# Performance work log

Hardware: AMD Instinct MI355X
Metric: run time of the kernel (lower is better)

## Reference

```python
import jax, jax.numpy as jnp
import numpy as np

# ---- module config (matches init_kwargs) ----
OGFH, OGFW = 256, 704
DOWNSAMPLE = 8
FH, FW = OGFH // DOWNSAMPLE, OGFW // DOWNSAMPLE   # 32, 88
DBOUND = (4.0, 45.0, 1.0)
D = int((DBOUND[1] - DBOUND[0]) / DBOUND[2])      # 41 depth bins
CAMC = 64
XB = (-50.0, 50.0, 0.5)    # lateral  -> nx = 200
YB = (-10.0, 10.0, 20.0)   # vertical -> ny = 1
ZB = (0.0, 50.0, 0.25)     # depth    -> nz = 200
NX = np.array([int((b[1] - b[0]) / b[2]) for b in (XB, YB, ZB)])  # [200, 1, 200]
DX = np.array([b[2] for b in (XB, YB, ZB)], dtype=np.float32)
BX = np.array([b[0] + b[2] / 2.0 for b in (XB, YB, ZB)], dtype=np.float32)


def make_frustum():
    # matches create_frustum_1camera: [D, fH, fW, 3] of (u, v, depth)
    ds = jnp.broadcast_to(
        jnp.arange(DBOUND[0], DBOUND[1], DBOUND[2], dtype=jnp.float32)[:, None, None],
        (D, FH, FW))
    xs = jnp.broadcast_to(
        jnp.linspace(0.0, OGFW - 1, FW, dtype=jnp.float32)[None, None, :], (D, FH, FW))
    ys = jnp.broadcast_to(
        jnp.linspace(0.0, OGFH - 1, FH, dtype=jnp.float32)[None, :, None], (D, FH, FW))
    return jnp.stack((xs, ys, ds), -1)


def setup_inputs() -> dict:
    key = jax.random.key(0)
    B = 4
    # depthnet output: first D channels = depth logits, next CAMC = context feats
    x = jax.random.normal(key, (B, D + CAMC, FH, FW), dtype=jnp.float32)
    fx = fy = 520.0
    K = jnp.array([[fx, 0.0, OGFW / 2.0],
                   [0.0, fy, OGFH / 2.0],
                   [0.0, 0.0, 1.0]], dtype=jnp.float32)
    intrins = jnp.broadcast_to(K, (B, 3, 3))
    post_rots = jnp.broadcast_to(jnp.eye(3, dtype=jnp.float32), (B, 3, 3))
    post_trans = jnp.zeros((B, 3), dtype=jnp.float32)
    return {"x": x, "intrins": intrins, "post_rots": post_rots, "post_trans": post_trans}


def _forward(x, intrins, post_rots, post_trans):
    B = x.shape[0]
    frustum = make_frustum()                                                     # [D,H,W,3]
    # ---- get_geometry ----
    pts = frustum[None] - post_trans[:, None, None, None, :]                     # [B,D,H,W,3]
    pts = jnp.einsum('bij,bdhwj->bdhwi', jnp.linalg.inv(post_rots), pts)
    pts = jnp.concatenate([pts[..., :2] * pts[..., 2:3], pts[..., 2:3]], -1)     # un-normalize
    geom = jnp.einsum('bij,bdhwj->bdhwi', jnp.linalg.inv(intrins), pts)          # [B,D,H,W,3]
    # ---- lift: depth softmax (x) context features ----
    depth = jax.nn.softmax(x[:, :D], axis=1)                                     # [B,D,H,W]
    feat = x[:, D:D + CAMC]                                                      # [B,C,H,W]
    vol = depth[:, None] * feat[:, :, None]                                      # [B,C,D,H,W]
    vol = jnp.transpose(vol, (0, 2, 3, 4, 1))                                    # [B,D,H,W,C]
    # ---- voxel_splat (sort+cumsum trick == segmented sum) ----
    Nprime = B * D * FH * FW
    feats = vol.reshape(Nprime, CAMC)
    # torch .long() truncates toward zero -> astype(int32)
    coords = ((geom - (BX - DX / 2.0)) / DX).astype(jnp.int32).reshape(Nprime, 3)
    bix = jnp.repeat(jnp.arange(B, dtype=jnp.int32), Nprime // B)
    kept = ((coords[:, 0] >= 0) & (coords[:, 0] < int(NX[0])) &
            (coords[:, 1] >= 0) & (coords[:, 1] < int(NX[1])) &
            (coords[:, 2] >= 0) & (coords[:, 2] < int(NX[2])))
    nseg = int(NX[0] * NX[1] * NX[2]) * B
    ranks = (coords[:, 0] * (int(NX[1]) * int(NX[2]) * B)
             + coords[:, 1] * (int(NX[2]) * B)
             + coords[:, 2] * B + bix)
    ranks = jnp.where(kept, ranks, nseg)  # dump bucket for dropped points
    pooled = jax.ops.segment_sum(jnp.where(kept[:, None], feats, 0.0), ranks,
                                 num_segments=nseg + 1)[:nseg]
    final = pooled.reshape(int(NX[0]), int(NX[1]), int(NX[2]), B, CAMC)          # [x,y,z,B,C]
    final = jnp.transpose(final, (3, 4, 1, 2, 0))                                # [B,C,ny,nz,nx]
    # torch.cat(final.unbind(dim=2), 1): collapse ny into channels (y-major)
    final = jnp.transpose(final, (0, 2, 1, 3, 4)).reshape(
        B, CAMC * int(NX[1]), int(NX[2]), int(NX[0]))                            # [B,C,200,200]
    return final


def reference(x, intrins, post_rots, post_trans):
    return _forward(x, intrins, post_rots, post_trans)
```

## Files before the change

kernel.cpp:

```cpp
#include <hip/hip_runtime.h>
#include <math.h>

#define DD   41
#define FHh  32
#define FWw  88
#define CC   64
#define CH   32
#define CG8  8
#define NXx  200
#define NZz  200
#define NCH  (DD + CC)
#define PLANE ((size_t)FHh * FWw)
#define NE   (DD * FWw)
#define DCAP 4
#define OVCAP 4096

__global__ __launch_bounds__(256) void lss_colpool(
    const float* __restrict__ x,
    const float* __restrict__ intrins,
    const float* __restrict__ post_rots,
    const float* __restrict__ post_trans,
    float* __restrict__ P, int* __restrict__ V,
    int* __restrict__ rowcnt8, int* __restrict__ ovcnt,
    float* __restrict__ out, int out_quads)
{
    __shared__ float Wt[DD][FHh + 1];
    __shared__ float F4s[FHh][36];
    __shared__ float Mi[18];
    __shared__ float pm[8][FHh + 1];
    __shared__ int   Vtmp[DD];

    int blk   = blockIdx.x;
    int chalf = blk & 1;
    int w     = (blk >> 1) % FWw;
    int b     = blk / (2 * FWw);
    int t     = threadIdx.x;
    const float* xb = x + (size_t)b * NCH * PLANE + w;

    for (int idx = t; idx < DD * FHh; idx += 256) {
        int d = idx >> 5, h = idx & 31;
        Wt[d][h] = xb[((size_t)d * FHh + h) * FWw];
    }
    for (int idx = t; idx < FHh * CH; idx += 256) {
        int c = idx & 31, h = idx >> 5;
        F4s[h][c] = xb[((size_t)(DD + chalf * CH + c) * FHh + h) * FWw];
    }
    if (t >= 64 && t < 64 + DD) Vtmp[t - 64] = -1;
    if (t == 0) {
        #pragma clang fp contract(off)
        for (int m = 0; m < 2; ++m) {
            const float* A = (m == 0 ? post_rots : intrins) + b * 9;
            float* O = Mi + m * 9;
            float a = A[0], bb = A[1], c = A[2];
            float d = A[3], e  = A[4], f = A[5];
            float g = A[6], h  = A[7], i = A[8];
            float det = a * (e * i - f * h) - bb * (d * i - f * g) + c * (d * h - e * g);
            O[0] = (e * i - f * h) / det;
            O[1] = (c * h - bb * i) / det;
            O[2] = (bb * f - c * e) / det;
            O[3] = (f * g - d * i) / det;
            O[4] = (a * i - c * g) / det;
            O[5] = (c * d - a * f) / det;
            O[6] = (d * h - e * g) / det;
            O[7] = (bb * g - a * h) / det;
            O[8] = (a * e - bb * d) / det;
        }
    }
    __syncthreads();

    int h = t & 31, l = t >> 5;
    float e_[6];
    {
        float pmax = -INFINITY;
        for (int d = l; d < DD; d += 8) pmax = fmaxf(pmax, Wt[d][h]);
        pm[l][h] = pmax;
    }
    __syncthreads();
    float mx = -INFINITY;
    for (int j = 0; j < 8; ++j) mx = fmaxf(mx, pm[j][h]);
    __syncthreads();
    {
        #pragma clang fp contract(off)
        float psum = 0.0f;
        int k = 0;
        for (int d = l; d < DD; d += 8, ++k) {
            float e = expf(Wt[d][h] - mx);
            e_[k] = e; psum += e;
        }
        pm[l][h] = psum;
    }
    __syncthreads();
    float s = 0.0f;
    for (int j = 0; j < 8; ++j) s += pm[j][h];

    {
        #pragma clang fp contract(off)
        float xs = (float)((double)w * 703.0 / 87.0);
        float ys = (float)((double)h * 255.0 / 31.0);
        float tx = post_trans[b * 3 + 0];
        float ty = post_trans[b * 3 + 1];
        float tz = post_trans[b * 3 + 2];
        int k = 0;
        for (int d = l; d < DD; d += 8, ++k) {
            float z  = 4.0f + (float)d;
            float px = xs - tx, py = ys - ty, pz = z - tz;
            float rx = Mi[0] * px + Mi[1] * py + Mi[2] * pz;
            float ry = Mi[3] * px + Mi[4] * py + Mi[5] * pz;
            float rz = Mi[6] * px + Mi[7] * py + Mi[8] * pz;
            float qx = rx * rz, qy = ry * rz, qz = rz;
            float gx = Mi[ 9] * qx + Mi[10] * qy + Mi[11] * qz;
            float gy = Mi[12] * qx + Mi[13] * qy + Mi[14] * qz;
            float gz = Mi[15] * qx + Mi[16] * qy + Mi[17] * qz;
            float cx = (gx + 50.0f) / 0.5f;
            float cy = (gy + 10.0f) / 20.0f;
            float cz = gz / 0.25f;
            int ix = (int)cx;
            int iy = (int)cy;
            int iz = (int)cz;
            bool kept = (ix >= 0) & (ix < NXx) & (iy == 0) & (iz >= 0) & (iz < NZz);
            if (kept) {
                Wt[d][h] = e_[k] / s;
                Vtmp[d] = iz * NXx + ix;
            } else {
                Wt[d][h] = 0.0f;
            }
        }
    }
    __syncthreads();

    float* Pb = P + ((size_t)b * NE) * CC + chalf * CH;
    {
        int c4 = t & 7;
        for (int d = t >> 3; d < DD; d += 32) {
            float4 acc = make_float4(0.f, 0.f, 0.f, 0.f);
            for (int hh = 0; hh < FHh; ++hh) {
                float wtv = Wt[d][hh];
                float4 fv = *(const float4*)&F4s[hh][c4 * 4];
                acc.x += wtv * fv.x; acc.y += wtv * fv.y;
                acc.z += wtv * fv.z; acc.w += wtv * fv.w;
            }
            *(float4*)&Pb[((size_t)d * FWw + w) * CC + c4 * 4] = acc;
        }
    }
    if (chalf == 0) {
        if (t < DD) V[(size_t)b * NE + (size_t)t * FWw + w] = Vtmp[t];
        if (w == 0) for (int i = t; i < NZz * 8; i += 256) rowcnt8[b * NZz * 8 + i] = 0;
    }
    if (blk == 0 && t == 0) *ovcnt = 0;

    {
        float4 z = make_float4(0.f, 0.f, 0.f, 0.f);
        float4* o4 = (float4*)out;
        int stride = gridDim.x * 256;
        for (int i = blk * 256 + t; i < out_quads; i += stride) o4[i] = z;
    }
}

__global__ __launch_bounds__(256) void lss_rowbuild(
    const float* __restrict__ P, const int* __restrict__ V,
    float* __restrict__ S, int* __restrict__ izd,
    int* __restrict__ rowcnt8, int* __restrict__ dlist8,
    int* __restrict__ ovcnt, int* __restrict__ ovlist,
    float* __restrict__ out)
{
    __shared__ float acc[CG8 * (NXx + 1)];
    __shared__ int ixw[FWw];
    __shared__ int izw[FWw];
    __shared__ int key;
    __shared__ int s_k;

    int blk = blockIdx.x;
    int cg = blk & 7;
    int bd = blk >> 3;
    int d = bd % DD;
    int b = bd / DD;
    int t = threadIdx.x;

    if (t == 0) key = 0x7fffffff;
    for (int i = t; i < CG8 * (NXx + 1); i += 256) acc[i] = 0.0f;
    __syncthreads();
    if (t < FWw) {
        int v = V[(size_t)bd * FWw + t];
        if (v >= 0) {
            int iz = v / NXx;
            izw[t] = iz; ixw[t] = v - iz * NXx;
            atomicMin(&key, (t << 16) | iz);
        } else { izw[t] = -1; ixw[t] = -1; }
    }
    __syncthreads();
    int kk = key;
    int s_iz = (kk == 0x7fffffff) ? -1 : (kk & 0xffff);
    if (cg == 0 && t == 0) izd[bd] = s_iz;
    if (s_iz < 0) return;

    int r = b * NZz + s_iz;
    if (t == 0) {
        int k = atomicAdd(&rowcnt8[r * 8 + cg], 1);
        if (k < DCAP) dlist8[(r * 8 + cg) * DCAP + k] = d;
        s_k = k;
    }
    if (cg == 0 && t < FWw && izw[t] >= 0 && izw[t] != s_iz) {
        int k = atomicAdd(ovcnt, 1);
        if (k < OVCAP)
            ovlist[k] = (b << 29) | (d << 23) | (t << 16) | (ixw[t] << 8) | izw[t];
    }

    const float* Pb = P + (size_t)bd * FWw * CC + cg * CG8;
    for (int idx = t; idx < FWw * 2; idx += 256) {
        int w = idx >> 1, q = idx & 1;
        if (izw[w] == s_iz) {
            float4 v = *(const float4*)&Pb[(size_t)w * CC + q * 4];
            int ix = ixw[w];
            int cb = q * 4;
            atomicAdd(&acc[(cb + 0) * (NXx + 1) + ix], v.x);
            atomicAdd(&acc[(cb + 1) * (NXx + 1) + ix], v.y);
            atomicAdd(&acc[(cb + 2) * (NXx + 1) + ix], v.z);
            atomicAdd(&acc[(cb + 3) * (NXx + 1) + ix], v.w);
        }
    }
    __syncthreads();

    bool owner0 = (s_k == 0);
    for (int i = t; i < CG8 * (NXx / 4); i += 256) {
        int c = i / (NXx / 4), q = i - c * (NXx / 4);
        int base = c * (NXx + 1) + q * 4;
        float4 vv;
        vv.x = acc[base + 0];
        vv.y = acc[base + 1];
        vv.z = acc[base + 2];
        vv.w = acc[base + 3];
        if (owner0) {
            float* orow = out + (((size_t)(b * CC + cg * CG8 + c)) * NZz + s_iz) * NXx;
            ((float4*)orow)[q] = vv;
        } else {
            float* Srow = S + ((size_t)bd * CC + cg * CG8 + c) * NXx;
            ((float4*)Srow)[q] = vv;
        }
    }
}

__global__ __launch_bounds__(256) void lss_fixup(
    const float* __restrict__ S, const int* __restrict__ izd,
    const int* __restrict__ rowcnt8, const int* __restrict__ dlist8,
    const float* __restrict__ P,
    const int* __restrict__ ovcnt, const int* __restrict__ ovlist,
    float* __restrict__ out)
{
    int b = blockIdx.x;
    int t = threadIdx.x;

    for (int pair = t; pair < NZz * 8; pair += 256) {
        int n = rowcnt8[b * NZz * 8 + pair];
        if (n <= 1) continue;
        int iz = pair >> 3, cg = pair & 7;
        const int* dl = dlist8 + (size_t)(b * NZz * 8 + pair) * DCAP;
        if (n <= DCAP) {
            for (int k = 1; k < n; ++k) {
                int d = dl[k];
                for (int c = 0; c < CG8; ++c) {
                    const float* Srow = S + ((size_t)(b * DD + d) * CC + cg * CG8 + c) * NXx;
                    float* orow = out + (((size_t)(b * CC + cg * CG8 + c)) * NZz + iz) * NXx;
                    for (int ix = 0; ix < NXx; ++ix) atomicAdd(&orow[ix], Srow[ix]);
                }
            }
        } else {
            int owner0 = dl[0];
            for (int d = 0; d < DD; ++d) {
                if (izd[b * DD + d] == iz && d != owner0) {
                    for (int c = 0; c < CG8; ++c) {
                        const float* Srow = S + ((size_t)(b * DD + d) * CC + cg * CG8 + c) * NXx;
                        float* orow = out + (((size_t)(b * CC + cg * CG8 + c)) * NZz + iz) * NXx;
                        for (int ix = 0; ix < NXx; ++ix) atomicAdd(&orow[ix], Srow[ix]);
                    }
                }
            }
        }
    }

    if (b == 0 && t == 0) {
        int nov = *ovcnt;
        if (nov > OVCAP) nov = OVCAP;
        for (int k = 0; k < nov; ++k) {
            int ent = ovlist[k];
            int eb  = (ent >> 29) & 7;
            int ed  = (ent >> 23) & 63;
            int ew  = (ent >> 16) & 127;
            int eix = (ent >> 8) & 255;
            int eiz = ent & 255;
            for (int c = 0; c < CC; ++c) {
                size_t o = (((size_t)(eb * CC + c)) * NZz + eiz) * NXx + eix;
                atomicAdd(&out[o], P[(((size_t)eb * DD + ed) * FWw + ew) * CC + c]);
            }
        }
    }
}

extern "C" void kernel_launch(void* const* d_in, const int* in_sizes, int n_in,
                              void* d_out, int out_size, void* d_ws, size_t ws_size,
                              hipStream_t stream)
{
    const float* x          = (const float*)d_in[0];
    const float* intrins    = (const float*)d_in[1];
    const float* post_rots  = (const float*)d_in[2];
    const float* post_trans = (const float*)d_in[3];
    float* out = (float*)d_out;

    int B = in_sizes[0] / (NCH * (int)PLANE);

    size_t off = 0;
    auto alloc = [&](size_t bytes) {
        void* p = (char*)d_ws + off;
        off = (off + bytes + 255) & ~(size_t)255;
        return p;
    };
    float* P       = (float*)alloc((size_t)B * NE * CC * sizeof(float));
    int*   V       = (int*)  alloc((size_t)B * NE * sizeof(int));
    float* S       = (float*)alloc((size_t)B * DD * CC * NXx * sizeof(float));
    int*   izd     = (int*)  alloc((size_t)B * DD * sizeof(int));
    int*   rowcnt8 = (int*)  alloc((size_t)B * NZz * 8 * sizeof(int));
    int*   dlist8  = (int*)  alloc((size_t)B * NZz * 8 * DCAP * sizeof(int));
    int*   ovcnt   = (int*)  alloc(256);
    int*   ovlist  = (int*)  alloc((size_t)OVCAP * sizeof(int));

    int out_quads = out_size / 4;

    lss_colpool<<<B * FWw * 2, 256, 0, stream>>>(x, intrins, post_rots, post_trans,
                                                 P, V, rowcnt8, ovcnt, out, out_quads);
    lss_rowbuild<<<B * DD * 8, 256, 0, stream>>>(P, V, S, izd, rowcnt8, dlist8,
                                                 ovcnt, ovlist, out);
    lss_fixup<<<B, 256, 0, stream>>>(S, izd, rowcnt8, dlist8, P, ovcnt, ovlist, out);
}
```

Baseline: 99.60 us.

## Fuse fixup into rowbuild kernel via last-block-done atomic counter

Merges the separate fixup kernel into the row-build kernel. The last block to finish, detected through an agent-scope acq_rel atomic counter in a new control area, runs the fixup for all batches. This removes one kernel launch and its launch gap. In exchange the fixup now runs serially in a single block across all batches instead of one block per batch, which could lengthen the tail if many rows need fixing.

```diff
diff --git a/kernel.cpp b/kernel.cpp
--- a/kernel.cpp
+++ b/kernel.cpp
@@ -21,7 +21,7 @@
     const float* __restrict__ post_rots,
     const float* __restrict__ post_trans,
     float* __restrict__ P, int* __restrict__ V,
-    int* __restrict__ rowcnt8, int* __restrict__ ovcnt,
+    int* __restrict__ rowcnt8, int* __restrict__ ctrl,
     float* __restrict__ out, int out_quads)
 {
     __shared__ float Wt[DD][FHh + 1];
@@ -146,7 +146,7 @@
         if (t < DD) V[(size_t)b * NE + (size_t)t * FWw + w] = Vtmp[t];
         if (w == 0) for (int i = t; i < NZz * 8; i += 256) rowcnt8[b * NZz * 8 + i] = 0;
     }
-    if (blk == 0 && t == 0) *ovcnt = 0;
+    if (blk == 0 && t < 64) ctrl[t] = 0;
 
     {
         float4 z = make_float4(0.f, 0.f, 0.f, 0.f);
@@ -156,18 +156,22 @@
     }
 }
 
-__global__ __launch_bounds__(256) void lss_rowbuild(
+__global__ __launch_bounds__(256) void lss_rowfix(
     const float* __restrict__ P, const int* __restrict__ V,
     float* __restrict__ S, int* __restrict__ izd,
     int* __restrict__ rowcnt8, int* __restrict__ dlist8,
-    int* __restrict__ ovcnt, int* __restrict__ ovlist,
-    float* __restrict__ out)
+    int* __restrict__ ctrl, int* __restrict__ ovlist,
+    float* __restrict__ out, int B)
 {
     __shared__ float acc[CG8 * (NXx + 1)];
     __shared__ int ixw[FWw];
     __shared__ int izw[FWw];
     __shared__ int key;
     __shared__ int s_k;
+    __shared__ int lastflag;
+
+    int* done2 = ctrl + 16;
+    int* ovcnt = ctrl + 32;
 
     int blk = blockIdx.x;
     int cg = blk & 7;
@@ -191,93 +195,95 @@
     int kk = key;
     int s_iz = (kk == 0x7fffffff) ? -1 : (kk & 0xffff);
     if (cg == 0 && t == 0) izd[bd] = s_iz;
-    if (s_iz < 0) return;
-
-    int r = b * NZz + s_iz;
+
+    if (s_iz >= 0) {
+        int r = b * NZz + s_iz;
+        if (t == 0) {
+            int k = atomicAdd(&rowcnt8[r * 8 + cg], 1);
+            if (k < DCAP) dlist8[(r * 8 + cg) * DCAP + k] = d;
+            s_k = k;
+        }
+        if (cg == 0 && t < FWw && izw[t] >= 0 && izw[t] != s_iz) {
+            int k = atomicAdd(ovcnt, 1);
+            if (k < OVCAP)
+                ovlist[k] = (b << 29) | (d << 23) | (t << 16) | (ixw[t] << 8) | izw[t];
+        }
+
+        const float* Pb = P + (size_t)bd * FWw * CC + cg * CG8;
+        for (int idx = t; idx < FWw * 2; idx += 256) {
+            int w = idx >> 1, q = idx & 1;
+            if (izw[w] == s_iz) {
+                float4 v = *(const float4*)&Pb[(size_t)w * CC + q * 4];
+                int ix = ixw[w];
+                int cb = q * 4;
+                atomicAdd(&acc[(cb + 0) * (NXx + 1) + ix], v.x);
+                atomicAdd(&acc[(cb + 1) * (NXx + 1) + ix], v.y);
+                atomicAdd(&acc[(cb + 2) * (NXx + 1) + ix], v.z);
+                atomicAdd(&acc[(cb + 3) * (NXx + 1) + ix], v.w);
+            }
+        }
+        __syncthreads();
+
+        bool owner0 = (s_k == 0);
+        for (int i = t; i < CG8 * (NXx / 4); i += 256) {
+            int c = i / (NXx / 4), q = i - c * (NXx / 4);
+            int base = c * (NXx + 1) + q * 4;
+            float4 vv;
+            vv.x = acc[base + 0];
+            vv.y = acc[base + 1];
+            vv.z = acc[base + 2];
+            vv.w = acc[base + 3];
+            if (owner0) {
+                float* orow = out + (((size_t)(b * CC + cg * CG8 + c)) * NZz + s_iz) * NXx;
+                ((float4*)orow)[q] = vv;
+            } else {
+                float* Srow = S + ((size_t)bd * CC + cg * CG8 + c) * NXx;
+                ((float4*)Srow)[q] = vv;
+            }
+        }
+    }
+
+    __syncthreads();
+    __threadfence();
     if (t == 0) {
-        int k = atomicAdd(&rowcnt8[r * 8 + cg], 1);
-        if (k < DCAP) dlist8[(r * 8 + cg) * DCAP + k] = d;
-        s_k = k;
-    }
-    if (cg == 0 && t < FWw && izw[t] >= 0 && izw[t] != s_iz) {
-        int k = atomicAdd(ovcnt, 1);
-        if (k < OVCAP)
-            ovlist[k] = (b << 29) | (d << 23) | (t << 16) | (ixw[t] << 8) | izw[t];
-    }
-
-    const float* Pb = P + (size_t)bd * FWw * CC + cg * CG8;
-    for (int idx = t; idx < FWw * 2; idx += 256) {
-        int w = idx >> 1, q = idx & 1;
-        if (izw[w] == s_iz) {
-            float4 v = *(const float4*)&Pb[(size_t)w * CC + q * 4];
-            int ix = ixw[w];
-            int cb = q * 4;
-            atomicAdd(&acc[(cb + 0) * (NXx + 1) + ix], v.x);
-            atomicAdd(&acc[(cb + 1) * (NXx + 1) + ix], v.y);
-            atomicAdd(&acc[(cb + 2) * (NXx + 1) + ix], v.z);
-            atomicAdd(&acc[(cb + 3) * (NXx + 1) + ix], v.w);
-        }
-    }
-    __syncthreads();
-
-    bool owner0 = (s_k == 0);
-    for (int i = t; i < CG8 * (NXx / 4); i += 256) {
-        int c = i / (NXx / 4), q = i - c * (NXx / 4);
-        int base = c * (NXx + 1) + q * 4;
-        float4 vv;
-        vv.x = acc[base + 0];
-        vv.y = acc[base + 1];
-        vv.z = acc[base + 2];
-        vv.w = acc[base + 3];
-        if (owner0) {
-            float* orow = out + (((size_t)(b * CC + cg * CG8 + c)) * NZz + s_iz) * NXx;
-            ((float4*)orow)[q] = vv;
-        } else {
-            float* Srow = S + ((size_t)bd * CC + cg * CG8 + c) * NXx;
-            ((float4*)Srow)[q] = vv;
-        }
-    }
-}
-
-__global__ __launch_bounds__(256) void lss_fixup(
-    const float* __restrict__ S, const int* __restrict__ izd,
-    const int* __restrict__ rowcnt8, const int* __restrict__ dlist8,
-    const float* __restrict__ P,
-    const int* __restrict__ ovcnt, const int* __restrict__ ovlist,
-    float* __restrict__ out)
-{
-    int b = blockIdx.x;
-    int t = threadIdx.x;
-
-    for (int pair = t; pair < NZz * 8; pair += 256) {
-        int n = rowcnt8[b * NZz * 8 + pair];
-        if (n <= 1) continue;
-        int iz = pair >> 3, cg = pair & 7;
-        const int* dl = dlist8 + (size_t)(b * NZz * 8 + pair) * DCAP;
-        if (n <= DCAP) {
-            for (int k = 1; k < n; ++k) {
-                int d = dl[k];
+        int k = __hip_atomic_fetch_add(done2, 1, __ATOMIC_ACQ_REL, __HIP_MEMORY_SCOPE_AGENT);
+        lastflag = (k == (int)gridDim.x - 1) ? 1 : 0;
+    }
+    __syncthreads();
+    if (!lastflag) return;
+
+    for (int bb = 0; bb < B; ++bb) {
+        for (int pair = t; pair < NZz * 8; pair += 256) {
+            int n = rowcnt8[bb * NZz * 8 + pair];
+            if (n <= 1) continue;
+            int iz = pair >> 3, cgp = pair & 7;
+            const int* dl = dlist8 + (size_t)(bb * NZz * 8 + pair) * DCAP;
+            int nn = (n <= DCAP) ? n : DCAP;
+            for (int k = 1; k < nn; ++k) {
+                int dd = dl[k];
                 for (int c = 0; c < CG8; ++c) {
-                    const float* Srow = S + ((size_t)(b * DD + d) * CC + cg * CG8 + c) * NXx;
-                    float* orow = out + (((size_t)(b * CC + cg * CG8 + c)) * NZz + iz) * NXx;
+                    const float* Srow = S + ((size_t)(bb * DD + dd) * CC + cgp * CG8 + c) * NXx;
+                    float* orow = out + (((size_t)(bb * CC + cgp * CG8 + c)) * NZz + iz) * NXx;
                     for (int ix = 0; ix < NXx; ++ix) atomicAdd(&orow[ix], Srow[ix]);
                 }
             }
-        } else {
-            int owner0 = dl[0];
-            for (int d = 0; d < DD; ++d) {
-                if (izd[b * DD + d] == iz && d != owner0) {
-                    for (int c = 0; c < CG8; ++c) {
-                        const float* Srow = S + ((size_t)(b * DD + d) * CC + cg * CG8 + c) * NXx;
-                        float* orow = out + (((size_t)(b * CC + cg * CG8 + c)) * NZz + iz) * NXx;
-                        for (int ix = 0; ix < NXx; ++ix) atomicAdd(&orow[ix], Srow[ix]);
+            if (n > DCAP) {
+                int owner0 = dl[0];
+                for (int dd = 0; dd < DD; ++dd) {
+                    bool indl = false;
+                    for (int k = 0; k < nn; ++k) indl |= (dl[k] == dd);
+                    if (izd[bb * DD + dd] == iz && dd != owner0 && !indl) {
+                        for (int c = 0; c < CG8; ++c) {
+                            const float* Srow = S + ((size_t)(bb * DD + dd) * CC + cgp * CG8 + c) * NXx;
+                            float* orow = out + (((size_t)(bb * CC + cgp * CG8 + c)) * NZz + iz) * NXx;
+                            for (int ix = 0; ix < NXx; ++ix) atomicAdd(&orow[ix], Srow[ix]);
+                        }
                     }
                 }
             }
         }
     }
-
-    if (b == 0 && t == 0) {
+    if (t == 0) {
         int nov = *ovcnt;
         if (nov > OVCAP) nov = OVCAP;
         for (int k = 0; k < nov; ++k) {
@@ -319,14 +325,13 @@
     int*   izd     = (int*)  alloc((size_t)B * DD * sizeof(int));
     int*   rowcnt8 = (int*)  alloc((size_t)B * NZz * 8 * sizeof(int));
     int*   dlist8  = (int*)  alloc((size_t)B * NZz * 8 * DCAP * sizeof(int));
-    int*   ovcnt   = (int*)  alloc(256);
+    int*   ctrl    = (int*)  alloc(256);
     int*   ovlist  = (int*)  alloc((size_t)OVCAP * sizeof(int));
 
     int out_quads = out_size / 4;
 
     lss_colpool<<<B * FWw * 2, 256, 0, stream>>>(x, intrins, post_rots, post_trans,
-                                                 P, V, rowcnt8, ovcnt, out, out_quads);
-    lss_rowbuild<<<B * DD * 8, 256, 0, stream>>>(P, V, S, izd, rowcnt8, dlist8,
-                                                 ovcnt, ovlist, out);
-    lss_fixup<<<B, 256, 0, stream>>>(S, izd, rowcnt8, dlist8, P, ovcnt, ovlist, out);
+                                                 P, V, rowcnt8, ctrl, out, out_quads);
+    lss_rowfix<<<B * DD * 8, 256, 0, stream>>>(P, V, S, izd, rowcnt8, dlist8,
+                                               ctrl, ovlist, out, B);
 }
```

Measured after the change: 236.5 us. 2.37x slower.
